# Kernel tuning notes

Measured on AMD Instinct MI355X. Metric: run time of the kernel, lower is better.

Reference implementation:

```python
import jax, jax.numpy as jnp
import numpy as np

V, D, H, L, F, S, B = 32000, 1024, 16, 4, 4096, 1024, 2
THETA = 10000.0
EPS = 1e-5


def rmsnorm(x, w):
    # faithful to source: rms = sqrt(mean(x^2)) + eps (eps OUTSIDE the sqrt)
    rms = jnp.sqrt(jnp.mean(x * x, axis=-1, keepdims=True)) + EPS
    return (x / rms) * w


def rope(x, pos):
    # x: [B, H, S, dk]; rotate interleaved even/odd pairs
    dk = x.shape[-1]
    inv_freq = 1.0 / (THETA ** (jnp.arange(0, dk, 2, dtype=jnp.float32) / dk))
    ang = pos[:, None].astype(jnp.float32) * inv_freq[None, :]  # [S, dk/2]
    cos, sin = jnp.cos(ang), jnp.sin(ang)
    x1, x2 = x[..., ::2], x[..., 1::2]
    r1 = x1 * cos - x2 * sin
    r2 = x1 * sin + x2 * cos
    return jnp.stack([r1, r2], axis=-1).reshape(x.shape)


def setup_inputs() -> dict:
    key = jax.random.key(0)
    ks = jax.random.split(key, 12)
    s_attn = np.sqrt(2.0 / (D + D)).astype(np.float32)
    s_ffn = np.sqrt(2.0 / (F + D)).astype(np.float32)
    s_head = np.sqrt(2.0 / (V + D)).astype(np.float32)
    return {
        "token_ids": jax.random.randint(ks[0], (B, S), 0, V),
        "tok_emb": jax.random.normal(ks[1], (V, D), jnp.float32),
        "lm_head_w": jax.random.normal(ks[2], (V, D), jnp.float32) * s_head,
        "ln_final_w": jnp.ones((D,), jnp.float32),
        "q_w": jax.random.normal(ks[3], (L, D, D), jnp.float32) * s_attn,
        "k_w": jax.random.normal(ks[4], (L, D, D), jnp.float32) * s_attn,
        "v_w": jax.random.normal(ks[5], (L, D, D), jnp.float32) * s_attn,
        "o_w": jax.random.normal(ks[6], (L, D, D), jnp.float32) * s_attn,
        "ln1_w": jnp.ones((L, D), jnp.float32),
        "ln2_w": jnp.ones((L, D), jnp.float32),
        "w1": jax.random.normal(ks[7], (L, F, D), jnp.float32) * s_ffn,
        "w2": jax.random.normal(ks[8], (L, D, F), jnp.float32) * s_ffn,
        "w3": jax.random.normal(ks[9], (L, F, D), jnp.float32) * s_ffn,
    }


def reference(token_ids, tok_emb, lm_head_w, ln_final_w, q_w, k_w, v_w, o_w,
              ln1_w, ln2_w, w1, w2, w3):
    b, s = token_ids.shape
    dk = D // H
    scale = 1.0 / np.sqrt(dk).astype(np.float32)
    pos = jnp.arange(s)
    causal = jnp.tril(jnp.ones((s, s), dtype=bool))  # mask[i,j] = i >= j
    x = tok_emb[token_ids]  # [B, S, D]

    for l in range(L):
        # attention block with RoPE
        h = rmsnorm(x, ln1_w[l])
        q = (h @ q_w[l].T).reshape(b, s, H, dk).transpose(0, 2, 1, 3)
        k = (h @ k_w[l].T).reshape(b, s, H, dk).transpose(0, 2, 1, 3)
        v = (h @ v_w[l].T).reshape(b, s, H, dk).transpose(0, 2, 1, 3)
        q = rope(q, pos)
        k = rope(k, pos)
        scores = jnp.einsum('bhqd,bhkd->bhqk', q, k) * scale
        scores = jnp.where(causal, scores, -jnp.inf)
        attn = jax.nn.softmax(scores, axis=-1)
        o = jnp.einsum('bhqk,bhkd->bhqd', attn, v)
        o = o.transpose(0, 2, 1, 3).reshape(b, s, D)
        x = x + o @ o_w[l].T

        # SwiGLU FFN block
        h2 = rmsnorm(x, ln2_w[l])
        xw = h2 @ w1[l].T                       # [B, S, F]
        swish = xw * jax.nn.sigmoid(xw)
        x = x + (swish * (h2 @ w3[l].T)) @ w2[l].T

    x = rmsnorm(x, ln_final_w)
    return x @ lm_head_w.T  # logits [B, S, V]
```

## Files before the change

### kernel.cpp

```cpp
#include <hip/hip_runtime.h>
#include <math.h>

#define V_SZ 32000
#define D_SZ 1024
#define H_SZ 16
#define L_SZ 4
#define F_SZ 4096
#define S_SZ 1024
#define B_SZ 2
#define DK 64
#define NTOK (B_SZ * S_SZ)
#define NEG_INF -3.0e38f

typedef _Float16 half8 __attribute__((ext_vector_type(8)));
typedef _Float16 half4 __attribute__((ext_vector_type(4)));
typedef float floatx4 __attribute__((ext_vector_type(4)));

__device__ __forceinline__ void gload16(const void* g, void* l) {
    __builtin_amdgcn_global_load_lds(
        (const __attribute__((address_space(1))) unsigned int*)g,
        (__attribute__((address_space(3))) unsigned int*)l, 16, 0, 0);
}

__global__ __launch_bounds__(256) void f2h7(const float* __restrict__ sq,
                                            const float* __restrict__ sk,
                                            const float* __restrict__ sv,
                                            const float* __restrict__ so,
                                            const float* __restrict__ s1,
                                            const float* __restrict__ s3,
                                            const float* __restrict__ s2,
                                            _Float16* __restrict__ d,
                                            int nDD8, int nFD8) {
    const int i = blockIdx.x * 256 + threadIdx.x;
    const float* s;
    int off;
    if (i < 4 * nDD8) {
        const int sel = i / nDD8;
        off = i - sel * nDD8;
        s = sel == 0 ? sq : (sel == 1 ? sk : (sel == 2 ? sv : so));
    } else {
        const int j = i - 4 * nDD8;
        const int sel = j / nFD8;
        off = j - sel * nFD8;
        s = sel == 0 ? s1 : (sel == 1 ? s3 : s2);
    }
    const float4 a = ((const float4*)s)[2 * off];
    const float4 b = ((const float4*)s)[2 * off + 1];
    half8 h = {(_Float16)a.x, (_Float16)a.y, (_Float16)a.z, (_Float16)a.w,
               (_Float16)b.x, (_Float16)b.y, (_Float16)b.z, (_Float16)b.w};
    ((half8*)d)[i] = h;
}

__global__ __launch_bounds__(256) void f2h(const float* __restrict__ in,
                                           _Float16* __restrict__ out, int n8) {
    const int i = blockIdx.x * 256 + threadIdx.x;
    if (i >= n8) return;
    const float4 a = ((const float4*)in)[2 * i];
    const float4 b = ((const float4*)in)[2 * i + 1];
    half8 h = {(_Float16)a.x, (_Float16)a.y, (_Float16)a.z, (_Float16)a.w,
               (_Float16)b.x, (_Float16)b.y, (_Float16)b.z, (_Float16)b.w};
    ((half8*)out)[i] = h;
}

__global__ __launch_bounds__(256) void hmul(_Float16* __restrict__ a,
                                            const _Float16* __restrict__ b, int n8) {
    const int i = blockIdx.x * 256 + threadIdx.x;
    if (i >= n8) return;
    half8 x = ((half8*)a)[i];
    const half8 y = ((const half8*)b)[i];
#pragma unroll
    for (int j = 0; j < 8; ++j) x[j] = (_Float16)((float)x[j] * (float)y[j]);
    ((half8*)a)[i] = x;
}

__global__ __launch_bounds__(256) void embed_kernel(const int* __restrict__ ids,
                                                    const float* __restrict__ emb,
                                                    float* __restrict__ x) {
    const int row = blockIdx.x;
    const int id = ids[row];
    const float4* src = (const float4*)(emb + (size_t)id * D_SZ);
    float4* dst = (float4*)(x + (size_t)row * D_SZ);
    dst[threadIdx.x] = src[threadIdx.x];
}

__global__ __launch_bounds__(256) void rmsnorm_kernel(const float* __restrict__ x,
                                                      const float* __restrict__ w,
                                                      _Float16* __restrict__ out) {
    const int row = blockIdx.x;
    const int tid = threadIdx.x;
    const float4 v = ((const float4*)(x + (size_t)row * D_SZ))[tid];
    float ss = v.x * v.x + v.y * v.y + v.z * v.z + v.w * v.w;
#pragma unroll
    for (int off = 32; off > 0; off >>= 1) ss += __shfl_down(ss, off, 64);
    __shared__ float red[4];
    if ((tid & 63) == 0) red[tid >> 6] = ss;
    __syncthreads();
    const float tot = red[0] + red[1] + red[2] + red[3];
    const float inv = 1.0f / (sqrtf(tot * (1.0f / (float)D_SZ)) + 1e-5f);
    const float4 wv = ((const float4*)w)[tid];
    half4 o = {(_Float16)(v.x * inv * wv.x), (_Float16)(v.y * inv * wv.y),
               (_Float16)(v.z * inv * wv.z), (_Float16)(v.w * inv * wv.w)};
    ((half4*)(out + (size_t)row * D_SZ))[tid] = o;
}

template <int EPI, bool MFAST, int TM>
__global__ __launch_bounds__(256, 5) void hgemm(const _Float16* __restrict__ A,
                                                const _Float16* __restrict__ B,
                                                float* __restrict__ Cf,
                                                _Float16* Ch,
                                                const _Float16* AUXh,
                                                _Float16* Cq,
                                                _Float16* Ck,
                                                _Float16* Cv,
                                                int M, int N, int K) {
    constexpr int WN = (TM == 128) ? 2 : 4;
    constexpr int CW = 128 / WN;
    constexpr int FN = CW / 16;
    __shared__ __align__(16) _Float16 As[2][TM * 32];
    __shared__ __align__(16) _Float16 Bs[2][128 * 32];
    const int tid = threadIdx.x;
    const int lane = tid & 63;
    const int wave = tid >> 6;
    const int wr = (TM == 128) ? (wave >> 1) : 0;
    const int wc = (TM == 128) ? (wave & 1) : wave;
    const int l15 = lane & 15, g = lane >> 4;

    const int gm = M / TM, gn = N >> 7, nwg = gm * gn;
    const int orig = blockIdx.x;
    const int q8 = nwg >> 3, r8 = nwg & 7, xcd = orig & 7, j8 = orig >> 3;
    const int wgid = (xcd < r8 ? xcd * (q8 + 1) : r8 * (q8 + 1) + (xcd - r8) * q8) + j8;
    const int bm = MFAST ? (wgid % gm) : (wgid / gn);
    const int bn = MFAST ? (wgid / gm) : (wgid % gn);
    const int m0 = bm * TM, n0 = bn * 128;

    const int offA0 = wave * (TM * 16) + lane * 16;
    const int offA1 = offA0 + 1024;
    const int rA0 = offA0 >> 6, kA0 = offA0 & 63;
    const int rA1 = offA1 >> 6, kA1 = offA1 & 63;
    const int offB0 = wave * 2048 + lane * 16;
    const int offB1 = offB0 + 1024;
    const int rB0 = offB0 >> 6, kB0 = offB0 & 63;
    const int rB1 = offB1 >> 6, kB1 = offB1 & 63;
    const char* gA0 = (const char*)(A + (size_t)(m0 + rA0) * K) + kA0;
    const char* gA1 = (const char*)(A + (size_t)(m0 + rA1) * K) + kA1;
    const char* gB0 = (const char*)(B + (size_t)(n0 + rB0) * K) + kB0;
    const char* gB1 = (const char*)(B + (size_t)(n0 + rB1) * K) + kB1;

#define STAGE(buf)                                                     \
    do {                                                               \
        gload16(gA0, (char*)As[buf] + offA0);                          \
        if constexpr (TM == 128) gload16(gA1, (char*)As[buf] + offA1); \
        gload16(gB0, (char*)Bs[buf] + offB0);                          \
        gload16(gB1, (char*)Bs[buf] + offB1);                          \
        gA0 += 64; gA1 += 64; gB0 += 64; gB1 += 64;                    \
    } while (0)

    floatx4 acc[4][FN];
#pragma unroll
    for (int i = 0; i < 4; i++)
#pragma unroll
        for (int j = 0; j < FN; j++) acc[i][j] = 0;

    STAGE(0);
    __syncthreads();
    int cur = 0;
    for (int kk = 0; kk < K; kk += 32) {
        if (kk + 32 < K) STAGE(cur ^ 1);
        half8 aF[4], bF[FN];
#pragma unroll
        for (int i = 0; i < 4; i++)
            aF[i] = *(const half8*)&As[cur][(wr * 64 + i * 16 + l15) * 32 + g * 8];
#pragma unroll
        for (int j = 0; j < FN; j++)
            bF[j] = *(const half8*)&Bs[cur][(wc * CW + j * 16 + l15) * 32 + g * 8];
#pragma unroll
        for (int i = 0; i < 4; i++)
#pragma unroll
            for (int j = 0; j < FN; j++)
                acc[i][j] = __builtin_amdgcn_mfma_f32_16x16x32_f16(aF[i], bF[j], acc[i][j], 0, 0, 0);
        __syncthreads();
        cur ^= 1;
    }
#undef STAGE

    const int rb = m0 + wr * 64 + g * 4;
    const int cb = n0 + wc * CW + l15;
    if (EPI == 4) {
        const int sel = n0 >> 10;
        _Float16* Cx = sel == 0 ? Cq : (sel == 1 ? Ck : Cv);
        const int cb0 = cb - sel * 1024;
#pragma unroll
        for (int i = 0; i < 4; i++) {
#pragma unroll
            for (int e = 0; e < 4; e++) {
                const int row = rb + i * 16 + e;
                const int pos = row & (S_SZ - 1);
#pragma unroll
                for (int j = 0; j < FN; j++) {
                    float v = acc[i][j][e];
                    const int col = cb0 + j * 16;
                    if (sel < 2) {
                        const float pp = __shfl_xor(v, 1, 64);
                        const int pi = (col & 63) >> 1;
                        const float invf = exp2f((float)pi * -0.41524101186f);
                        float sn, cs;
                        sincosf((float)pos * invf, &sn, &cs);
                        v = (col & 1) ? (pp * sn + v * cs) : (v * cs - pp * sn);
                    }
                    Cx[(size_t)row * 1024 + col] = (_Float16)v;
                }
            }
        }
        return;
    }
#pragma unroll
    for (int i = 0; i < 4; i++) {
#pragma unroll
        for (int e = 0; e < 4; e++) {
            const int row = rb + i * 16 + e;
#pragma unroll
            for (int j = 0; j < FN; j++) {
                const float v = acc[i][j][e];
                const int col = cb + j * 16;
                if (EPI == 0) {
                    Cf[(size_t)row * N + col] = v;
                } else if (EPI == 1) {
                    Cf[(size_t)row * N + col] += v;
                } else if (EPI == 2) {
                    Ch[(size_t)row * N + col] =
                        (_Float16)(v / (1.0f + __expf(-v)));
                } else if (EPI == 3) {
                    const size_t idx = (size_t)row * N + col;
                    Ch[idx] = (_Float16)((float)AUXh[idx] * v);
                } else if (EPI == 5) {
                    if (col < 4096)
                        Ch[(size_t)row * 4096 + col] =
                            (_Float16)(v / (1.0f + __expf(-v)));
                    else
                        Cq[(size_t)row * 4096 + col - 4096] = (_Float16)v;
                }
            }
        }
    }
}

__global__ __launch_bounds__(256) void vtrans(const _Float16* __restrict__ vh,
                                              _Float16* __restrict__ vt) {
    __shared__ __align__(16) _Float16 Ls[64][80];
    const int t = threadIdx.x;
    const int s0 = blockIdx.x * 64;
    const int bh = blockIdx.y;
    const int b = bh >> 4, h = bh & 15;
#pragma unroll
    for (int p = 0; p < 2; ++p) {
        const int sl = p * 32 + (t >> 3);
        const int d = (t & 7) * 8;
        *(half8*)&Ls[sl][d] =
            *(const half8*)&vh[((size_t)b * S_SZ + s0 + sl) * D_SZ + h * 64 + d];
    }
    __syncthreads();
#pragma unroll
    for (int p = 0; p < 2; ++p) {
        const int d = p * 32 + (t >> 3);
        const int sc = (t & 7) * 8;
        half8 v;
#pragma unroll
        for (int j = 0; j < 8; ++j) v[j] = Ls[sc + j][d];
        *(half8*)&vt[((size_t)bh * 64 + d) * S_SZ + s0 + sc] = v;
    }
}

__global__ __launch_bounds__(256) void attn_mfma(const _Float16* __restrict__ qh,
                                                 const _Float16* __restrict__ kh,
                                                 const _Float16* __restrict__ vt,
                                                 _Float16* __restrict__ o) {
    __shared__ __align__(16) _Float16 Ks[2][64 * 64];
    __shared__ __align__(16) _Float16 Vs[2][64 * 64];
    __shared__ __align__(16) _Float16 Ps[4][16][88];
    const int tid = threadIdx.x;
    const int lane = tid & 63, wave = tid >> 6;
    const int l15 = lane & 15, g = lane >> 4;
    const int bx = blockIdx.x;
    const int bh = blockIdx.y;
    const int h = bh & 15;
    const size_t tokb = (size_t)(bh >> 4) * S_SZ;

    const int qt0 = bx, qt1 = 15 - bx;
    const int qb0 = qt0 * 64, qb1 = qt1 * 64;
    const int ktmax = qt1;

    const int qrow = l15 * 4 + wave;
    half8 qA0[2], qA1[2];
#pragma unroll
    for (int kk = 0; kk < 2; ++kk) {
        qA0[kk] = *(const half8*)&qh[(tokb + qb0 + qrow) * D_SZ + h * 64 + kk * 32 + g * 8];
        qA1[kk] = *(const half8*)&qh[(tokb + qb1 + qrow) * D_SZ + h * 64 + kk * 32 + g * 8];
    }

    floatx4 accO0[4], accO1[4];
#pragma unroll
    for (int s = 0; s < 4; s++) { accO0[s] = 0; accO1[s] = 0; }
    float m0_[4] = {NEG_INF, NEG_INF, NEG_INF, NEG_INF};
    float l0_[4] = {0.0f, 0.0f, 0.0f, 0.0f};
    float m1_[4] = {NEG_INF, NEG_INF, NEG_INF, NEG_INF};
    float l1_[4] = {0.0f, 0.0f, 0.0f, 0.0f};

    const char* KbB = (const char*)(kh + tokb * D_SZ + h * 64);
    const char* VbB = (const char*)(vt + (size_t)bh * 64 * S_SZ);
    const int so0 = wave * 2048 + lane * 16;
    const int so1 = so0 + 1024;
    const int r0 = so0 >> 7, c0 = (so0 >> 4) & 7;
    const int r1 = so1 >> 7, c1 = (so1 >> 4) & 7;
    const int gc0 = ((c0 ^ (r0 & 7)) << 4);
    const int gc1 = ((c1 ^ (r1 & 7)) << 4);

#define STAGEKV(buf, kt)                                                   \
    do {                                                                   \
        const size_t kvr = (size_t)(kt) * 64;                              \
        gload16(KbB + (kvr + r0) * 2048 + gc0, (char*)Ks[buf] + so0);      \
        gload16(KbB + (kvr + r1) * 2048 + gc1, (char*)Ks[buf] + so1);      \
        gload16(VbB + r0 * 2048 + kvr * 2 + gc0, (char*)Vs[buf] + so0);    \
        gload16(VbB + r1 * 2048 + kvr * 2 + gc1, (char*)Vs[buf] + so1);    \
    } while (0)

#define LDSW(arr, rr, cc) \
    (*(const half8*)&(arr)[(rr) * 64 + ((((cc) ^ ((rr) & 7))) << 3)])

    auto computeTile = [&](const half8* qA, floatx4* accO, float* m_, float* l_,
                           int qbase, int kt, bool diag, int buf) {
        const int kv0 = kt * 64;
        floatx4 accS[4];
        __builtin_amdgcn_s_setprio(1);
#pragma unroll
        for (int sub = 0; sub < 4; ++sub) {
            accS[sub] = 0;
#pragma unroll
            for (int kk = 0; kk < 2; ++kk) {
                half8 kB = LDSW(Ks[buf], sub * 16 + l15, kk * 4 + g);
                accS[sub] = __builtin_amdgcn_mfma_f32_16x16x32_f16(qA[kk], kB, accS[sub], 0, 0, 0);
            }
        }
        __builtin_amdgcn_s_setprio(0);
        float sv[4][4];
        float mx[4] = {NEG_INF, NEG_INF, NEG_INF, NEG_INF};
#pragma unroll
        for (int sub = 0; sub < 4; ++sub)
#pragma unroll
            for (int e = 0; e < 4; ++e) {
                float s = accS[sub][e] * 0.125f;
                if (diag && (kv0 + sub * 16 + l15 > qbase + (g * 4 + e) * 4 + wave))
                    s = NEG_INF;
                sv[sub][e] = s;
                mx[e] = fmaxf(mx[e], s);
            }
#pragma unroll
        for (int msk = 1; msk <= 8; msk <<= 1)
#pragma unroll
            for (int e = 0; e < 4; ++e)
                mx[e] = fmaxf(mx[e], __shfl_xor(mx[e], msk, 64));
        float sf[4];
#pragma unroll
        for (int e = 0; e < 4; ++e) {
            const float mn = fmaxf(m_[e], mx[e]);
            sf[e] = __expf(m_[e] - mn);
            m_[e] = mn;
        }
        float rs[4] = {0.0f, 0.0f, 0.0f, 0.0f};
#pragma unroll
        for (int sub = 0; sub < 4; ++sub)
#pragma unroll
            for (int e = 0; e < 4; ++e) {
                const float p = __expf(sv[sub][e] - m_[e]);
                sv[sub][e] = p;
                rs[e] += p;
            }
#pragma unroll
        for (int msk = 1; msk <= 8; msk <<= 1)
#pragma unroll
            for (int e = 0; e < 4; ++e)
                rs[e] += __shfl_xor(rs[e], msk, 64);
#pragma unroll
        for (int e = 0; e < 4; ++e) l_[e] = l_[e] * sf[e] + rs[e];
#pragma unroll
        for (int sub = 0; sub < 4; ++sub)
#pragma unroll
            for (int e = 0; e < 4; ++e) accO[sub][e] *= sf[e];
#pragma unroll
        for (int sub = 0; sub < 4; ++sub)
#pragma unroll
            for (int e = 0; e < 4; ++e)
                Ps[wave][g * 4 + e][sub * 16 + l15] = (_Float16)sv[sub][e];
        half8 aP[2];
        aP[0] = *(const half8*)&Ps[wave][l15][g * 8];
        aP[1] = *(const half8*)&Ps[wave][l15][32 + g * 8];
        __builtin_amdgcn_s_setprio(1);
#pragma unroll
        for (int sub = 0; sub < 4; ++sub)
#pragma unroll
            for (int kk = 0; kk < 2; ++kk) {
                half8 vB = LDSW(Vs[buf], sub * 16 + l15, kk * 4 + g);
                accO[sub] = __builtin_amdgcn_mfma_f32_16x16x32_f16(aP[kk], vB, accO[sub], 0, 0, 0);
            }
        __builtin_amdgcn_s_setprio(0);
    };

    STAGEKV(0, 0);
    __syncthreads();
    int cur = 0;
    for (int kt = 0; kt <= ktmax; ++kt) {
        if (kt < ktmax) STAGEKV(cur ^ 1, kt + 1);
        computeTile(qA1, accO1, m1_, l1_, qb1, kt, kt == qt1, cur);
        if (kt <= qt0)
            computeTile(qA0, accO0, m0_, l0_, qb0, kt, kt == qt0, cur);
        __syncthreads();
        cur ^= 1;
    }
#undef STAGEKV
#undef LDSW

#pragma unroll
    for (int sub = 0; sub < 4; ++sub)
#pragma unroll
        for (int e = 0; e < 4; ++e) {
            const int rr = (g * 4 + e) * 4 + wave;
            o[(tokb + qb1 + rr) * D_SZ + h * 64 + sub * 16 + l15] =
                (_Float16)(accO1[sub][e] / l1_[e]);
            o[(tokb + qb0 + rr) * D_SZ + h * 64 + sub * 16 + l15] =
                (_Float16)(accO0[sub][e] / l0_[e]);
        }
}

extern "C" void kernel_launch(void* const* d_in, const int* in_sizes, int n_in,
                              void* d_out, int out_size, void* d_ws, size_t ws_size,
                              hipStream_t stream) {
    const int*   token_ids  = (const int*)d_in[0];
    const float* tok_emb    = (const float*)d_in[1];
    const float* lm_head_w  = (const float*)d_in[2];
    const float* ln_final_w = (const float*)d_in[3];
    const float* q_w        = (const float*)d_in[4];
    const float* k_w        = (const float*)d_in[5];
    const float* v_w        = (const float*)d_in[6];
    const float* o_w        = (const float*)d_in[7];
    const float* ln1_w      = (const float*)d_in[8];
    const float* ln2_w      = (const float*)d_in[9];
    const float* w1         = (const float*)d_in[10];
    const float* w2         = (const float*)d_in[11];
    const float* w3         = (const float*)d_in[12];
    float* out = (float*)d_out;

    char* W = (char*)d_ws;
    const size_t MB = 1u << 20;
    float*    x    = (float*)(W + 0);
    _Float16* h    = (_Float16*)(W + 8 * MB);
    _Float16* ao   = (_Float16*)(W + 12 * MB);
    _Float16* wq   = (_Float16*)(W + 16 * MB);
    _Float16* wo   = wq + 3 * (1u << 20);
    _Float16* ww1  = (_Float16*)(W + 24 * MB);
    _Float16* ww2  = ww1 + 2 * (F_SZ * D_SZ);
    _Float16* qh   = (_Float16*)(W + 48 * MB);
    _Float16* kh   = (_Float16*)(W + 52 * MB);
    _Float16* vh   = (_Float16*)(W + 56 * MB);
    _Float16* vt   = (_Float16*)(W + 60 * MB);
    _Float16* ff3h = (_Float16*)(W + 48 * MB);
    _Float16* ff1h = (_Float16*)(W + 64 * MB);
    _Float16* whead = (_Float16*)(W + 24 * MB);

    embed_kernel<<<NTOK, 256, 0, stream>>>(token_ids, tok_emb, x);

    const int nDD8 = D_SZ * D_SZ / 8;
    const int nFD8 = F_SZ * D_SZ / 8;
    const int nCNV = 4 * nDD8 + 3 * nFD8;
    const dim3 gQKV(3 * D_SZ / 128 * (NTOK / 128));
    const dim3 gD64(D_SZ / 128 * (NTOK / 64));
    const dim3 gW13(2 * F_SZ / 128 * (NTOK / 128));
    const dim3 gATT(S_SZ / 128, B_SZ * H_SZ);
    const dim3 gVT(S_SZ / 64, B_SZ * H_SZ);

    for (int l = 0; l < L_SZ; l++) {
        const size_t oDD = (size_t)l * D_SZ * D_SZ;
        const size_t oFD = (size_t)l * F_SZ * D_SZ;
        rmsnorm_kernel<<<NTOK, 256, 0, stream>>>(x, ln1_w + (size_t)l * D_SZ, h);
        f2h7<<<nCNV / 256, 256, 0, stream>>>(q_w + oDD, k_w + oDD, v_w + oDD,
                                             o_w + oDD, w1 + oFD, w3 + oFD,
                                             w2 + oFD, wq, nDD8, nFD8);
        hgemm<4, true, 128><<<gQKV, 256, 0, stream>>>(h, wq, nullptr, nullptr, nullptr,
                                                      qh, kh, vh, NTOK, 3 * D_SZ, D_SZ);
        vtrans<<<gVT, 256, 0, stream>>>(vh, vt);
        attn_mfma<<<gATT, 256, 0, stream>>>(qh, kh, vt, ao);
        hgemm<1, false, 64><<<gD64, 256, 0, stream>>>(ao, wo, x, nullptr, nullptr,
                                                      nullptr, nullptr, nullptr, NTOK, D_SZ, D_SZ);
        rmsnorm_kernel<<<NTOK, 256, 0, stream>>>(x, ln2_w + (size_t)l * D_SZ, h);
        hgemm<5, true, 128><<<gW13, 256, 0, stream>>>(h, ww1, nullptr, ff1h, nullptr,
                                                      ff3h, nullptr, nullptr, NTOK, 2 * F_SZ, D_SZ);
        hmul<<<NTOK * F_SZ / 8 / 256, 256, 0, stream>>>(ff1h, ff3h, NTOK * F_SZ / 8);
        hgemm<1, false, 64><<<gD64, 256, 0, stream>>>(ff1h, ww2, x, nullptr, nullptr,
                                                      nullptr, nullptr, nullptr, NTOK, D_SZ, F_SZ);
    }
    rmsnorm_kernel<<<NTOK, 256, 0, stream>>>(x, ln_final_w, h);
    const int nVD8 = V_SZ * D_SZ / 8;
    f2h<<<(nVD8 + 255) / 256, 256, 0, stream>>>(lm_head_w, whead, nVD8);
    const dim3 gOUT(V_SZ / 128 * (NTOK / 128));
    hgemm<0, true, 128><<<gOUT, 256, 0, stream>>>(h, whead, out, nullptr, nullptr,
                                                  nullptr, nullptr, nullptr, NTOK, V_SZ, D_SZ);
}
```

Measured before the change: 1.244 ms.

## Fuse W1/W3 GEMMs with SwiGLU gating into a dual-accumulator kernel

Replaces the concatenated W1|W3 GEMM (writing SiLU output and the W3 output to separate fp16 buffers) and the following elementwise multiply kernel with a single kernel. It accumulates both products for the same output tile and applies silu(a)*b in the epilogue. This removes one launch and the write and re-read of two [2048x4096] fp16 intermediates. It also drops the occupancy hint of 5 from the hgemm launch bounds, and the new kernel uses a 64-row tile with twice the accumulator registers, which may reduce occupancy.

After: 1.242 ms. Within noise of the previous version (-0.2%).

```diff
diff --git a/kernel.cpp b/kernel.cpp
--- a/kernel.cpp
+++ b/kernel.cpp
@@ -62,17 +62,6 @@
     ((half8*)out)[i] = h;
 }
 
-__global__ __launch_bounds__(256) void hmul(_Float16* __restrict__ a,
-                                            const _Float16* __restrict__ b, int n8) {
-    const int i = blockIdx.x * 256 + threadIdx.x;
-    if (i >= n8) return;
-    half8 x = ((half8*)a)[i];
-    const half8 y = ((const half8*)b)[i];
-#pragma unroll
-    for (int j = 0; j < 8; ++j) x[j] = (_Float16)((float)x[j] * (float)y[j]);
-    ((half8*)a)[i] = x;
-}
-
 __global__ __launch_bounds__(256) void embed_kernel(const int* __restrict__ ids,
                                                     const float* __restrict__ emb,
                                                     float* __restrict__ x) {
@@ -104,15 +93,15 @@
 }
 
 template <int EPI, bool MFAST, int TM>
-__global__ __launch_bounds__(256, 5) void hgemm(const _Float16* __restrict__ A,
-                                                const _Float16* __restrict__ B,
-                                                float* __restrict__ Cf,
-                                                _Float16* Ch,
-                                                const _Float16* AUXh,
-                                                _Float16* Cq,
-                                                _Float16* Ck,
-                                                _Float16* Cv,
-                                                int M, int N, int K) {
+__global__ __launch_bounds__(256) void hgemm(const _Float16* __restrict__ A,
+                                             const _Float16* __restrict__ B,
+                                             float* __restrict__ Cf,
+                                             _Float16* Ch,
+                                             const _Float16* AUXh,
+                                             _Float16* Cq,
+                                             _Float16* Ck,
+                                             _Float16* Cv,
+                                             int M, int N, int K) {
     constexpr int WN = (TM == 128) ? 2 : 4;
     constexpr int CW = 128 / WN;
     constexpr int FN = CW / 16;
@@ -232,13 +221,99 @@
                 } else if (EPI == 3) {
                     const size_t idx = (size_t)row * N + col;
                     Ch[idx] = (_Float16)((float)AUXh[idx] * v);
-                } else if (EPI == 5) {
-                    if (col < 4096)
-                        Ch[(size_t)row * 4096 + col] =
-                            (_Float16)(v / (1.0f + __expf(-v)));
-                    else
-                        Cq[(size_t)row * 4096 + col - 4096] = (_Float16)v;
                 }
+            }
+        }
+    }
+}
+
+__global__ __launch_bounds__(256) void hgemm_ff(const _Float16* __restrict__ A,
+                                                const _Float16* __restrict__ B1,
+                                                const _Float16* __restrict__ B3,
+                                                _Float16* __restrict__ Ch,
+                                                int M, int N, int K) {
+    __shared__ __align__(16) _Float16 As[2][64 * 32];
+    __shared__ __align__(16) _Float16 Bs1[2][128 * 32];
+    __shared__ __align__(16) _Float16 Bs3[2][128 * 32];
+    const int tid = threadIdx.x;
+    const int lane = tid & 63;
+    const int wave = tid >> 6;
+    const int l15 = lane & 15, g = lane >> 4;
+
+    const int gm = M >> 6, gn = N >> 7, nwg = gm * gn;
+    const int orig = blockIdx.x;
+    const int q8 = nwg >> 3, r8 = nwg & 7, xcd = orig & 7, j8 = orig >> 3;
+    const int wgid = (xcd < r8 ? xcd * (q8 + 1) : r8 * (q8 + 1) + (xcd - r8) * q8) + j8;
+    const int bm = wgid % gm, bn = wgid / gm;
+    const int m0 = bm * 64, n0 = bn * 128;
+
+    const int offA = wave * 1024 + lane * 16;
+    const int rA = offA >> 6, kA = offA & 63;
+    const int offB0 = wave * 2048 + lane * 16;
+    const int offB1 = offB0 + 1024;
+    const int rB0 = offB0 >> 6, kB0 = offB0 & 63;
+    const int rB1 = offB1 >> 6, kB1 = offB1 & 63;
+    const char* gA  = (const char*)(A  + (size_t)(m0 + rA) * K) + kA;
+    const char* gB10 = (const char*)(B1 + (size_t)(n0 + rB0) * K) + kB0;
+    const char* gB11 = (const char*)(B1 + (size_t)(n0 + rB1) * K) + kB1;
+    const char* gB30 = (const char*)(B3 + (size_t)(n0 + rB0) * K) + kB0;
+    const char* gB31 = (const char*)(B3 + (size_t)(n0 + rB1) * K) + kB1;
+
+#define STAGEF(buf)                                   \
+    do {                                              \
+        gload16(gA,   (char*)As[buf]  + offA);        \
+        gload16(gB10, (char*)Bs1[buf] + offB0);       \
+        gload16(gB11, (char*)Bs1[buf] + offB1);       \
+        gload16(gB30, (char*)Bs3[buf] + offB0);       \
+        gload16(gB31, (char*)Bs3[buf] + offB1);       \
+        gA += 64; gB10 += 64; gB11 += 64;             \
+        gB30 += 64; gB31 += 64;                       \
+    } while (0)
+
+    floatx4 acc1[4][2], acc3[4][2];
+#pragma unroll
+    for (int i = 0; i < 4; i++)
+#pragma unroll
+        for (int j = 0; j < 2; j++) { acc1[i][j] = 0; acc3[i][j] = 0; }
+
+    STAGEF(0);
+    __syncthreads();
+    int cur = 0;
+    for (int kk = 0; kk < K; kk += 32) {
+        if (kk + 32 < K) STAGEF(cur ^ 1);
+        half8 aF[4], b1F[2], b3F[2];
+#pragma unroll
+        for (int i = 0; i < 4; i++)
+            aF[i] = *(const half8*)&As[cur][(i * 16 + l15) * 32 + g * 8];
+#pragma unroll
+        for (int j = 0; j < 2; j++) {
+            b1F[j] = *(const half8*)&Bs1[cur][(wave * 32 + j * 16 + l15) * 32 + g * 8];
+            b3F[j] = *(const half8*)&Bs3[cur][(wave * 32 + j * 16 + l15) * 32 + g * 8];
+        }
+#pragma unroll
+        for (int i = 0; i < 4; i++)
+#pragma unroll
+            for (int j = 0; j < 2; j++) {
+                acc1[i][j] = __builtin_amdgcn_mfma_f32_16x16x32_f16(aF[i], b1F[j], acc1[i][j], 0, 0, 0);
+                acc3[i][j] = __builtin_amdgcn_mfma_f32_16x16x32_f16(aF[i], b3F[j], acc3[i][j], 0, 0, 0);
+            }
+        __syncthreads();
+        cur ^= 1;
+    }
+#undef STAGEF
+
+    const int cb = n0 + wave * 32 + l15;
+#pragma unroll
+    for (int i = 0; i < 4; i++) {
+#pragma unroll
+        for (int e = 0; e < 4; e++) {
+            const int row = m0 + i * 16 + g * 4 + e;
+#pragma unroll
+            for (int j = 0; j < 2; j++) {
+                const float v1 = acc1[i][j][e];
+                const float v3 = acc3[i][j][e];
+                const float sw = v1 / (1.0f + __expf(-v1));
+                Ch[(size_t)row * N + cb + j * 16] = (_Float16)(sw * v3);
             }
         }
     }
@@ -456,12 +531,12 @@
     _Float16* wq   = (_Float16*)(W + 16 * MB);
     _Float16* wo   = wq + 3 * (1u << 20);
     _Float16* ww1  = (_Float16*)(W + 24 * MB);
-    _Float16* ww2  = ww1 + 2 * (F_SZ * D_SZ);
+    _Float16* ww3  = ww1 + (size_t)F_SZ * D_SZ;
+    _Float16* ww2  = ww1 + 2 * (size_t)F_SZ * D_SZ;
     _Float16* qh   = (_Float16*)(W + 48 * MB);
     _Float16* kh   = (_Float16*)(W + 52 * MB);
     _Float16* vh   = (_Float16*)(W + 56 * MB);
     _Float16* vt   = (_Float16*)(W + 60 * MB);
-    _Float16* ff3h = (_Float16*)(W + 48 * MB);
     _Float16* ff1h = (_Float16*)(W + 64 * MB);
     _Float16* whead = (_Float16*)(W + 24 * MB);
 
@@ -472,7 +547,7 @@
     const int nCNV = 4 * nDD8 + 3 * nFD8;
     const dim3 gQKV(3 * D_SZ / 128 * (NTOK / 128));
     const dim3 gD64(D_SZ / 128 * (NTOK / 64));
-    const dim3 gW13(2 * F_SZ / 128 * (NTOK / 128));
+    const dim3 gFF(F_SZ / 128 * (NTOK / 64));
     const dim3 gATT(S_SZ / 128, B_SZ * H_SZ);
     const dim3 gVT(S_SZ / 64, B_SZ * H_SZ);
 
@@ -490,9 +565,7 @@
         hgemm<1, false, 64><<<gD64, 256, 0, stream>>>(ao, wo, x, nullptr, nullptr,
                                                       nullptr, nullptr, nullptr, NTOK, D_SZ, D_SZ);
         rmsnorm_kernel<<<NTOK, 256, 0, stream>>>(x, ln2_w + (size_t)l * D_SZ, h);
-        hgemm<5, true, 128><<<gW13, 256, 0, stream>>>(h, ww1, nullptr, ff1h, nullptr,
-                                                      ff3h, nullptr, nullptr, NTOK, 2 * F_SZ, D_SZ);
-        hmul<<<NTOK * F_SZ / 8 / 256, 256, 0, stream>>>(ff1h, ff3h, NTOK * F_SZ / 8);
+        hgemm_ff<<<gFF, 256, 0, stream>>>(h, ww1, ww3, ff1h, NTOK, F_SZ, D_SZ);
         hgemm<1, false, 64><<<gD64, 256, 0, stream>>>(ff1h, ww2, x, nullptr, nullptr,
                                                       nullptr, nullptr, nullptr, NTOK, D_SZ, F_SZ);
     }
```
